# Kernel tuning notes

Measured on AMD Instinct MI355X. Metric: run time of the kernel, lower is better.

The kernel has to match this reference:

```python
import jax, jax.numpy as jnp
import numpy as np

HIDDEN = 1024
HEADS = 16
HEAD_DIM = HIDDEN // HEADS


def setup_inputs() -> dict:
    key = jax.random.key(0)
    ks = jax.random.split(key, 8)
    B, S = 2, 2048
    scale = 1.0 / np.sqrt(HIDDEN)
    inp = {
        "hidden_states": jax.random.normal(ks[0], (B, S, HIDDEN), dtype=jnp.float32),
        "attention_mask": jnp.zeros((B, 1, 1, S), dtype=jnp.float32),
        "q_w": jax.random.normal(ks[1], (HIDDEN, HIDDEN), dtype=jnp.float32) * scale,
        "q_b": jnp.zeros((HIDDEN,), dtype=jnp.float32),
        "k_w": jax.random.normal(ks[2], (HIDDEN, HIDDEN), dtype=jnp.float32) * scale,
        "k_b": jnp.zeros((HIDDEN,), dtype=jnp.float32),
        "v_w": jax.random.normal(ks[3], (HIDDEN, HIDDEN), dtype=jnp.float32) * scale,
        "v_b": jnp.zeros((HIDDEN,), dtype=jnp.float32),
    }
    return inp


def _split_heads(x):
    # [B, S, H] -> [B, heads, S, head_dim]
    B, S, _ = x.shape
    return x.reshape(B, S, HEADS, HEAD_DIM).transpose(0, 2, 1, 3)


def reference(hidden_states, attention_mask, q_w, q_b, k_w, k_b, v_w, v_b):
    # Linear projections (torch Linear: x @ W.T + b; here weights stored as [in, out])
    q = _split_heads(hidden_states @ q_w + q_b)  # [B, h, S, d]
    k = _split_heads(hidden_states @ k_w + k_b)
    v = _split_heads(hidden_states @ v_w + v_b)

    scores = jnp.einsum("bhqd,bhkd->bhqk", q, k) / jnp.sqrt(jnp.float32(HEAD_DIM))
    scores = scores + attention_mask  # additive mask, broadcast [B,1,1,S]
    probs = jax.nn.softmax(scores, axis=-1)
    # dropout prob = 0.0 -> identity
    ctx = jnp.einsum("bhqk,bhkd->bhqd", probs, v)  # [B, h, S, d]
    B, _, S, _ = ctx.shape
    ctx = ctx.transpose(0, 2, 1, 3).reshape(B, S, HIDDEN)
    return ctx
```

## Files before the change

### kernel.cpp

```cpp
#include <hip/hip_runtime.h>

typedef __bf16 bf16;
typedef __attribute__((ext_vector_type(8))) __bf16 bf16x8;
typedef __attribute__((ext_vector_type(4))) __bf16 bf16x4;
typedef __attribute__((ext_vector_type(4))) float f32x4;
typedef __attribute__((ext_vector_type(2))) unsigned int uint2v;
typedef __attribute__((ext_vector_type(4))) unsigned int uint4v;

#define MFMA(a, b, c) __builtin_amdgcn_mfma_f32_16x16x32_bf16((a), (b), (c), 0, 0, 0)
#define LOG2E 1.44269504088896340736f

__device__ __forceinline__ bf16x8 cvt8(float4 a, float4 b) {
  bf16x8 r;
  r[0] = (bf16)a.x; r[1] = (bf16)a.y; r[2] = (bf16)a.z; r[3] = (bf16)a.w;
  r[4] = (bf16)b.x; r[5] = (bf16)b.y; r[6] = (bf16)b.z; r[7] = (bf16)b.w;
  return r;
}

__device__ __forceinline__ void stage16(const bf16* g, bf16* l) {
  __builtin_amdgcn_global_load_lds(
      (const __attribute__((address_space(1))) void*)g,
      (__attribute__((address_space(3))) void*)l, 16, 0, 0);
}

__global__ __launch_bounds__(256)
void cvt(const float* __restrict__ hs, const float* __restrict__ qw,
         const float* __restrict__ kw, const float* __restrict__ vw,
         bf16* __restrict__ Xb, bf16* __restrict__ Wt) {
  const int bid = blockIdx.x, tid = threadIdx.x;
  if (bid < 2048) {
    size_t off = (size_t)bid * 2048 + tid * 8;
    float4 x0 = *(const float4*)(hs + off);
    float4 x1 = *(const float4*)(hs + off + 4);
    *(bf16x8*)(Xb + off) = cvt8(x0, x1);
  } else {
    int t = bid - 2048;
    int z = t >> 8, ti = t & 255;
    const float* W = (z == 0) ? qw : (z == 1) ? kw : vw;
    int k0 = (ti >> 4) * 64, n0 = (ti & 15) * 64;
    __shared__ bf16 T[64 * 72];
    #pragma unroll
    for (int i = 0; i < 16; ++i) {
      int e = i * 256 + tid;
      int kr = e >> 6, nc = e & 63;
      T[nc * 72 + kr] = (bf16)W[(size_t)(k0 + kr) * 1024 + n0 + nc];
    }
    __syncthreads();
    #pragma unroll
    for (int i = 0; i < 2; ++i) {
      int e = i * 256 + tid;
      int nr = e >> 3, kg = e & 7;
      *(bf16x8*)(Wt + (size_t)z * 1048576 + (size_t)(n0 + nr) * 1024 + k0 + kg * 8) =
          *(const bf16x8*)&T[nr * 72 + kg * 8];
    }
  }
}

__global__ __launch_bounds__(256, 3)
void qkv_gemm(const bf16* __restrict__ Xb, const bf16* __restrict__ Wt,
              const float* __restrict__ qbias, const float* __restrict__ kbias,
              const float* __restrict__ vbias,
              bf16* __restrict__ qo, bf16* __restrict__ ko, bf16* __restrict__ vo) {
  const int blk = blockIdx.x;
  const int xcd = blk & 7, slot = blk >> 3;
  const int mb = xcd * 4 + slot / 24;
  const int nb = slot % 24;
  const int z = nb >> 3, nbm = nb & 7;
  const bf16* W = Wt + (size_t)z * 1048576;

  const int tid = threadIdx.x;
  const int wave = tid >> 6, lane = tid & 63, quad = lane >> 4, c = lane & 15;
  const int wr = wave >> 1, wc = wave & 1;
  const int lrow = lane >> 3;
  const int lg = (lane & 7) ^ lrow;

  __shared__ bf16 As[128 * 64];
  __shared__ bf16 Bs[128 * 64];

  f32x4 acc[4][4] = {};

  for (int k0 = 0; k0 < 1024; k0 += 64) {
    #pragma unroll
    for (int i = 0; i < 4; ++i) {
      int r = wave * 32 + i * 8;
      stage16(Xb + (size_t)(mb * 128 + r + lrow) * 1024 + k0 + lg * 8, &As[r * 64]);
      stage16(W + (size_t)(nbm * 128 + r + lrow) * 1024 + k0 + lg * 8, &Bs[r * 64]);
    }
    __syncthreads();
    #pragma unroll
    for (int ch = 0; ch < 2; ++ch) {
      bf16x8 af[4];
      #pragma unroll
      for (int rt = 0; rt < 4; ++rt) {
        int row = wr * 64 + rt * 16 + c;
        af[rt] = *(const bf16x8*)&As[row * 64 + ((((ch << 2) | quad) ^ (c & 7)) << 3)];
      }
      #pragma unroll
      for (int nt = 0; nt < 4; ++nt) {
        int row = wc * 64 + nt * 16 + c;
        bf16x8 bfrag = *(const bf16x8*)&Bs[row * 64 + ((((ch << 2) | quad) ^ (c & 7)) << 3)];
        #pragma unroll
        for (int rt = 0; rt < 4; ++rt)
          acc[rt][nt] = MFMA(af[rt], bfrag, acc[rt][nt]);
      }
    }
    __syncthreads();
  }

  const float* bias = (z == 0) ? qbias : (z == 1) ? kbias : vbias;
  float bv[4];
  #pragma unroll
  for (int nt = 0; nt < 4; ++nt)
    bv[nt] = bias[nbm * 128 + wc * 64 + nt * 16 + c];

  if (z == 2) {
    #pragma unroll
    for (int rt = 0; rt < 4; ++rt)
      #pragma unroll
      for (int nt = 0; nt < 4; ++nt) {
        int m0 = mb * 128 + wr * 64 + rt * 16 + 4 * quad;
        int n = nbm * 128 + wc * 64 + nt * 16 + c;
        bf16x4 pk;
        #pragma unroll
        for (int reg = 0; reg < 4; ++reg) pk[reg] = (bf16)(acc[rt][nt][reg] + bv[nt]);
        int b = m0 >> 11, s0 = m0 & 2047, h = n >> 6, d = n & 63;
        *(bf16x4*)&vo[(((size_t)b * 16 + h) * 64 + d) * 2048 + s0] = pk;
      }
  } else {
    bf16* dst = (z == 0) ? qo : ko;
    const float scale = (z == 0) ? 0.125f * LOG2E : 1.0f;
    #pragma unroll
    for (int rt = 0; rt < 4; ++rt)
      #pragma unroll
      for (int nt = 0; nt < 4; ++nt)
        #pragma unroll
        for (int reg = 0; reg < 4; ++reg) {
          float v = (acc[rt][nt][reg] + bv[nt]) * scale;
          int m = mb * 128 + wr * 64 + rt * 16 + 4 * quad + reg;
          int n = nbm * 128 + wc * 64 + nt * 16 + c;
          int b = m >> 11, s = m & 2047, h = n >> 6, d = n & 63;
          dst[(((size_t)b * 16 + h) * 2048 + s) * 64 + d] = (bf16)v;
        }
  }
}

__global__ __launch_bounds__(256, 4)
void attn(const bf16* __restrict__ qg, const bf16* __restrict__ kg,
          const bf16* __restrict__ vtg, const float* __restrict__ mask,
          float* __restrict__ out) {
  const int blk = blockIdx.x;
  const int xcd = blk & 7, slot = blk >> 3;
  const int bh = xcd * 4 + (slot >> 5);
  const int qblk = slot & 31;
  const int b = bh >> 4, h = bh & 15;
  const int tid = threadIdx.x;
  const int wave = tid >> 6, lane = tid & 63, quad = lane >> 4, c = lane & 15;
  const int w2 = wave & 1;
  const int wq = wave >> 1;
  const int lrow = lane >> 3, lg = (lane & 7) ^ lrow;

  __shared__ __align__(16) unsigned char SH[40960];
  float* Ms = (float*)(SH + 32768);

  const bf16* qb_ = qg + (size_t)bh * 2048 * 64;
  const bf16* kb_ = kg + (size_t)bh * 2048 * 64;
  const bf16* vb_ = vtg + (size_t)bh * 64 * 2048;

  #pragma unroll
  for (int i = 0; i < 2; ++i) {
    int idx = i * 1024 + tid * 4;
    float4 m = *(const float4*)&mask[b * 2048 + idx];
    float4 ms = {m.x * LOG2E, m.y * LOG2E, m.z * LOG2E, m.w * LOG2E};
    *(float4*)&Ms[idx] = ms;
  }

  bf16x8 qf[2][2];
  #pragma unroll
  for (int g = 0; g < 2; ++g)
    #pragma unroll
    for (int ch = 0; ch < 2; ++ch)
      qf[g][ch] = *(const bf16x8*)(qb_ +
          (size_t)(qblk * 64 + wq * 32 + g * 16 + c) * 64 + ch * 32 + quad * 8);

  #pragma unroll
  for (int i = 0; i < 2; ++i) {
    int r = wave * 16 + i * 8;
    stage16(kb_ + (size_t)(r + lrow) * 64 + lg * 8, (bf16*)SH + r * 64);
    stage16(vb_ + (size_t)(r + lrow) * 2048 + lg * 8, (bf16*)(SH + 16384) + r * 64);
  }
  __asm__ volatile("s_waitcnt lgkmcnt(0)" ::: "memory");

  f32x4 o[4][2] = {};
  float lsum[2] = {0.f, 0.f};

  for (int kt = 0; kt < 32; ++kt) {
    const int cur = kt & 1;
    bf16* Kc = (bf16*)(SH + cur * 8192);
    bf16* Vc = (bf16*)(SH + 16384 + cur * 8192);
    __asm__ volatile("s_waitcnt vmcnt(0)" ::: "memory");
    __builtin_amdgcn_s_barrier();
    __builtin_amdgcn_sched_barrier(0);

    if (kt < 31) {
      bf16* Kn = (bf16*)(SH + (cur ^ 1) * 8192);
      bf16* Vn = (bf16*)(SH + 16384 + (cur ^ 1) * 8192);
      #pragma unroll
      for (int i = 0; i < 2; ++i) {
        int r = wave * 16 + i * 8;
        stage16(kb_ + (size_t)((kt + 1) * 64 + r + lrow) * 64 + lg * 8, Kn + r * 64);
        stage16(vb_ + (size_t)(r + lrow) * 2048 + (kt + 1) * 64 + lg * 8, Vn + r * 64);
      }
    }
    __builtin_amdgcn_sched_barrier(0);

    f32x4 s[2][2];
    #pragma unroll
    for (int kt2 = 0; kt2 < 2; ++kt2) {
      float4 mv = *(const float4*)&Ms[kt * 64 + w2 * 32 + kt2 * 16 + 4 * quad];
      f32x4 sv = {mv.x, mv.y, mv.z, mv.w};
      s[0][kt2] = sv;
      s[1][kt2] = sv;
    }

    __builtin_amdgcn_s_setprio(1);
    #pragma unroll
    for (int kt2 = 0; kt2 < 2; ++kt2)
      #pragma unroll
      for (int ch = 0; ch < 2; ++ch) {
        bf16x8 kf = *(const bf16x8*)&Kc[(w2 * 32 + kt2 * 16 + c) * 64 +
                                        ((((ch << 2) | quad) ^ (c & 7)) << 3)];
        s[0][kt2] = MFMA(kf, qf[0][ch], s[0][kt2]);
        s[1][kt2] = MFMA(kf, qf[1][ch], s[1][kt2]);
      }
    __builtin_amdgcn_s_setprio(0);

    bf16x8 pf[2];
    #pragma unroll
    for (int g = 0; g < 2; ++g) {
      unsigned int A0, A1, B0, B1;
      {
        bf16x4 pk;
        #pragma unroll
        for (int reg = 0; reg < 4; ++reg) {
          float p = __builtin_amdgcn_exp2f(s[g][0][reg]);
          lsum[g] += p;
          pk[reg] = (bf16)p;
        }
        uint2v uu = __builtin_bit_cast(uint2v, pk);
        A0 = uu.x; A1 = uu.y;
      }
      {
        bf16x4 pk;
        #pragma unroll
        for (int reg = 0; reg < 4; ++reg) {
          float p = __builtin_amdgcn_exp2f(s[g][1][reg]);
          lsum[g] += p;
          pk[reg] = (bf16)p;
        }
        uint2v uu = __builtin_bit_cast(uint2v, pk);
        B0 = uu.x; B1 = uu.y;
      }
      __asm__ volatile("v_permlane32_swap_b32 %0, %1" : "+v"(A0), "+v"(B0));
      __asm__ volatile("v_permlane32_swap_b32 %0, %1" : "+v"(A1), "+v"(B1));
      __asm__ volatile("v_permlane16_swap_b32 %0, %1" : "+v"(A0), "+v"(B0));
      __asm__ volatile("v_permlane16_swap_b32 %0, %1" : "+v"(A1), "+v"(B1));
      uint4v up = {A0, A1, B0, B1};
      pf[g] = __builtin_bit_cast(bf16x8, up);
    }

    __builtin_amdgcn_s_setprio(1);
    #pragma unroll
    for (int dt = 0; dt < 4; ++dt) {
      bf16x8 vf = *(const bf16x8*)&Vc[(dt * 16 + c) * 64 +
                                      ((((w2 << 2) | quad) ^ (c & 7)) << 3)];
      o[dt][0] = MFMA(vf, pf[0], o[dt][0]);
      o[dt][1] = MFMA(vf, pf[1], o[dt][1]);
    }
    __builtin_amdgcn_s_setprio(0);
  }

  #pragma unroll
  for (int g = 0; g < 2; ++g) {
    lsum[g] += __shfl_xor(lsum[g], 16, 64);
    lsum[g] += __shfl_xor(lsum[g], 32, 64);
  }

  __syncthreads();
  float* rec = (float*)(SH + (size_t)(wq * 64 + lane) * 144);
  if (w2 == 1) {
    #pragma unroll
    for (int dt = 0; dt < 4; ++dt)
      #pragma unroll
      for (int g = 0; g < 2; ++g)
        *(f32x4*)&rec[(dt * 2 + g) * 4] = o[dt][g];
    rec[32] = lsum[0];
    rec[33] = lsum[1];
  }
  __syncthreads();
  if (w2 == 0) {
    float inv[2];
    #pragma unroll
    for (int g = 0; g < 2; ++g) inv[g] = 1.0f / (lsum[g] + rec[32 + g]);
    #pragma unroll
    for (int dt = 0; dt < 4; ++dt)
      #pragma unroll
      for (int g = 0; g < 2; ++g) {
        f32x4 po = *(const f32x4*)&rec[(dt * 2 + g) * 4];
        const int srow = qblk * 64 + wq * 32 + g * 16 + c;
        float4 st = { (o[dt][g][0] + po[0]) * inv[g],
                      (o[dt][g][1] + po[1]) * inv[g],
                      (o[dt][g][2] + po[2]) * inv[g],
                      (o[dt][g][3] + po[3]) * inv[g] };
        *(float4*)&out[((size_t)b * 2048 + srow) * 1024 + h * 64 + dt * 16 + 4 * quad] = st;
      }
  }
}

extern "C" void kernel_launch(void* const* d_in, const int* in_sizes, int n_in,
                              void* d_out, int out_size, void* d_ws, size_t ws_size,
                              hipStream_t stream) {
  const float* hs   = (const float*)d_in[0];
  const float* mask = (const float*)d_in[1];
  const float* qw   = (const float*)d_in[2];
  const float* qb   = (const float*)d_in[3];
  const float* kw   = (const float*)d_in[4];
  const float* kb   = (const float*)d_in[5];
  const float* vw   = (const float*)d_in[6];
  const float* vb   = (const float*)d_in[7];
  float* out = (float*)d_out;

  bf16* Xb   = (bf16*)d_ws;
  bf16* Wt   = Xb + (size_t)4096 * 1024;
  bf16* q_ws = Wt + (size_t)3 * 1048576;
  bf16* k_ws = q_ws + (size_t)4096 * 1024;
  bf16* v_ws = k_ws + (size_t)4096 * 1024;

  cvt<<<dim3(2816), 256, 0, stream>>>(hs, qw, kw, vw, Xb, Wt);
  qkv_gemm<<<dim3(768), 256, 0, stream>>>(Xb, Wt, qb, kb, vb, q_ws, k_ws, v_ws);
  attn<<<dim3(1024), 256, 0, stream>>>(q_ws, k_ws, v_ws, mask, out);
}
```

Baseline: 161.3 us.

## Load K/V fragments straight from global into registers, drop LDS staging

Rewrites the attention kernel so each wave loads its K, V and mask fragments directly from global memory into registers, double-buffered in two register sets, with no LDS staging or barriers. Each wave now covers all keys for 32 query rows, which removes the split-K reduction through shared memory, and the grid is halved to 512 blocks of 128 query rows each. The aim is to remove barrier and LDS traffic. The cost is that each wave re-reads K/V from global/L2 with no sharing across the block, plus higher register pressure and fewer blocks in flight.

```diff
diff --git a/kernel.cpp b/kernel.cpp
--- a/kernel.cpp
+++ b/kernel.cpp
@@ -144,35 +144,28 @@
   }
 }
 
-__global__ __launch_bounds__(256, 4)
+struct Frags {
+  bf16x8 k[4];
+  bf16x8 v[4];
+  float4 m[2];
+};
+
+__global__ __launch_bounds__(256, 1)
 void attn(const bf16* __restrict__ qg, const bf16* __restrict__ kg,
           const bf16* __restrict__ vtg, const float* __restrict__ mask,
           float* __restrict__ out) {
   const int blk = blockIdx.x;
-  const int xcd = blk & 7, slot = blk >> 3;
-  const int bh = xcd * 4 + (slot >> 5);
-  const int qblk = slot & 31;
+  const int xcd = blk & 7;
+  const int bh = xcd * 4 + ((blk >> 3) & 3);
+  const int qsup = blk >> 5;
   const int b = bh >> 4, h = bh & 15;
   const int tid = threadIdx.x;
   const int wave = tid >> 6, lane = tid & 63, quad = lane >> 4, c = lane & 15;
-  const int w2 = wave & 1;
-  const int wq = wave >> 1;
-  const int lrow = lane >> 3, lg = (lane & 7) ^ lrow;
-
-  __shared__ __align__(16) unsigned char SH[40960];
-  float* Ms = (float*)(SH + 32768);
 
   const bf16* qb_ = qg + (size_t)bh * 2048 * 64;
   const bf16* kb_ = kg + (size_t)bh * 2048 * 64;
   const bf16* vb_ = vtg + (size_t)bh * 64 * 2048;
-
-  #pragma unroll
-  for (int i = 0; i < 2; ++i) {
-    int idx = i * 1024 + tid * 4;
-    float4 m = *(const float4*)&mask[b * 2048 + idx];
-    float4 ms = {m.x * LOG2E, m.y * LOG2E, m.z * LOG2E, m.w * LOG2E};
-    *(float4*)&Ms[idx] = ms;
-  }
+  const float* mb_ = mask + (size_t)b * 2048;
 
   bf16x8 qf[2][2];
   #pragma unroll
@@ -180,60 +173,47 @@
     #pragma unroll
     for (int ch = 0; ch < 2; ++ch)
       qf[g][ch] = *(const bf16x8*)(qb_ +
-          (size_t)(qblk * 64 + wq * 32 + g * 16 + c) * 64 + ch * 32 + quad * 8);
-
-  #pragma unroll
-  for (int i = 0; i < 2; ++i) {
-    int r = wave * 16 + i * 8;
-    stage16(kb_ + (size_t)(r + lrow) * 64 + lg * 8, (bf16*)SH + r * 64);
-    stage16(vb_ + (size_t)(r + lrow) * 2048 + lg * 8, (bf16*)(SH + 16384) + r * 64);
-  }
-  __asm__ volatile("s_waitcnt lgkmcnt(0)" ::: "memory");
+          (size_t)(qsup * 128 + wave * 32 + g * 16 + c) * 64 + ch * 32 + quad * 8);
 
   f32x4 o[4][2] = {};
   float lsum[2] = {0.f, 0.f};
 
-  for (int kt = 0; kt < 32; ++kt) {
-    const int cur = kt & 1;
-    bf16* Kc = (bf16*)(SH + cur * 8192);
-    bf16* Vc = (bf16*)(SH + 16384 + cur * 8192);
-    __asm__ volatile("s_waitcnt vmcnt(0)" ::: "memory");
-    __builtin_amdgcn_s_barrier();
-    __builtin_amdgcn_sched_barrier(0);
-
-    if (kt < 31) {
-      bf16* Kn = (bf16*)(SH + (cur ^ 1) * 8192);
-      bf16* Vn = (bf16*)(SH + 16384 + (cur ^ 1) * 8192);
-      #pragma unroll
-      for (int i = 0; i < 2; ++i) {
-        int r = wave * 16 + i * 8;
-        stage16(kb_ + (size_t)((kt + 1) * 64 + r + lrow) * 64 + lg * 8, Kn + r * 64);
-        stage16(vb_ + (size_t)(r + lrow) * 2048 + (kt + 1) * 64 + lg * 8, Vn + r * 64);
-      }
-    }
-    __builtin_amdgcn_sched_barrier(0);
-
+  Frags fA, fB;
+
+  auto LOADF = [&](Frags& f, int kt) {
+    #pragma unroll
+    for (int kt2 = 0; kt2 < 2; ++kt2)
+      #pragma unroll
+      for (int ch = 0; ch < 2; ++ch)
+        f.k[kt2 * 2 + ch] = *(const bf16x8*)(kb_ +
+            (size_t)(kt * 32 + kt2 * 16 + c) * 64 + (ch * 4 + quad) * 8);
+    #pragma unroll
+    for (int dt = 0; dt < 4; ++dt)
+      f.v[dt] = *(const bf16x8*)(vb_ +
+          (size_t)(dt * 16 + c) * 2048 + kt * 32 + quad * 8);
+    #pragma unroll
+    for (int kt2 = 0; kt2 < 2; ++kt2)
+      f.m[kt2] = *(const float4*)(mb_ + kt * 32 + kt2 * 16 + 4 * quad);
+  };
+
+  auto COMPUTE = [&](const Frags& f) {
     f32x4 s[2][2];
     #pragma unroll
     for (int kt2 = 0; kt2 < 2; ++kt2) {
-      float4 mv = *(const float4*)&Ms[kt * 64 + w2 * 32 + kt2 * 16 + 4 * quad];
-      f32x4 sv = {mv.x, mv.y, mv.z, mv.w};
+      f32x4 sv = {f.m[kt2].x * LOG2E, f.m[kt2].y * LOG2E,
+                  f.m[kt2].z * LOG2E, f.m[kt2].w * LOG2E};
       s[0][kt2] = sv;
       s[1][kt2] = sv;
     }
-
     __builtin_amdgcn_s_setprio(1);
     #pragma unroll
     for (int kt2 = 0; kt2 < 2; ++kt2)
       #pragma unroll
       for (int ch = 0; ch < 2; ++ch) {
-        bf16x8 kf = *(const bf16x8*)&Kc[(w2 * 32 + kt2 * 16 + c) * 64 +
-                                        ((((ch << 2) | quad) ^ (c & 7)) << 3)];
-        s[0][kt2] = MFMA(kf, qf[0][ch], s[0][kt2]);
-        s[1][kt2] = MFMA(kf, qf[1][ch], s[1][kt2]);
+        s[0][kt2] = MFMA(f.k[kt2 * 2 + ch], qf[0][ch], s[0][kt2]);
+        s[1][kt2] = MFMA(f.k[kt2 * 2 + ch], qf[1][ch], s[1][kt2]);
       }
     __builtin_amdgcn_s_setprio(0);
-
     bf16x8 pf[2];
     #pragma unroll
     for (int g = 0; g < 2; ++g) {
@@ -267,52 +247,36 @@
       uint4v up = {A0, A1, B0, B1};
       pf[g] = __builtin_bit_cast(bf16x8, up);
     }
-
     __builtin_amdgcn_s_setprio(1);
     #pragma unroll
     for (int dt = 0; dt < 4; ++dt) {
-      bf16x8 vf = *(const bf16x8*)&Vc[(dt * 16 + c) * 64 +
-                                      ((((w2 << 2) | quad) ^ (c & 7)) << 3)];
-      o[dt][0] = MFMA(vf, pf[0], o[dt][0]);
-      o[dt][1] = MFMA(vf, pf[1], o[dt][1]);
+      o[dt][0] = MFMA(f.v[dt], pf[0], o[dt][0]);
+      o[dt][1] = MFMA(f.v[dt], pf[1], o[dt][1]);
     }
     __builtin_amdgcn_s_setprio(0);
+  };
+
+  LOADF(fA, 0);
+  for (int kt = 0; kt < 64; kt += 2) {
+    LOADF(fB, kt + 1);
+    COMPUTE(fA);
+    if (kt + 2 < 64) LOADF(fA, kt + 2);
+    COMPUTE(fB);
   }
 
   #pragma unroll
   for (int g = 0; g < 2; ++g) {
-    lsum[g] += __shfl_xor(lsum[g], 16, 64);
-    lsum[g] += __shfl_xor(lsum[g], 32, 64);
-  }
-
-  __syncthreads();
-  float* rec = (float*)(SH + (size_t)(wq * 64 + lane) * 144);
-  if (w2 == 1) {
-    #pragma unroll
-    for (int dt = 0; dt < 4; ++dt)
-      #pragma unroll
-      for (int g = 0; g < 2; ++g)
-        *(f32x4*)&rec[(dt * 2 + g) * 4] = o[dt][g];
-    rec[32] = lsum[0];
-    rec[33] = lsum[1];
-  }
-  __syncthreads();
-  if (w2 == 0) {
-    float inv[2];
-    #pragma unroll
-    for (int g = 0; g < 2; ++g) inv[g] = 1.0f / (lsum[g] + rec[32 + g]);
-    #pragma unroll
-    for (int dt = 0; dt < 4; ++dt)
-      #pragma unroll
-      for (int g = 0; g < 2; ++g) {
-        f32x4 po = *(const f32x4*)&rec[(dt * 2 + g) * 4];
-        const int srow = qblk * 64 + wq * 32 + g * 16 + c;
-        float4 st = { (o[dt][g][0] + po[0]) * inv[g],
-                      (o[dt][g][1] + po[1]) * inv[g],
-                      (o[dt][g][2] + po[2]) * inv[g],
-                      (o[dt][g][3] + po[3]) * inv[g] };
-        *(float4*)&out[((size_t)b * 2048 + srow) * 1024 + h * 64 + dt * 16 + 4 * quad] = st;
-      }
+    float l = lsum[g];
+    l += __shfl_xor(l, 16, 64);
+    l += __shfl_xor(l, 32, 64);
+    const float inv = 1.0f / l;
+    const int srow = qsup * 128 + wave * 32 + g * 16 + c;
+    #pragma unroll
+    for (int dt = 0; dt < 4; ++dt) {
+      float4 st = { o[dt][g][0] * inv, o[dt][g][1] * inv,
+                    o[dt][g][2] * inv, o[dt][g][3] * inv };
+      *(float4*)&out[((size_t)b * 2048 + srow) * 1024 + h * 64 + dt * 16 + 4 * quad] = st;
+    }
   }
 }
 
@@ -337,5 +301,5 @@
 
   cvt<<<dim3(2816), 256, 0, stream>>>(hs, qw, kw, vw, Xb, Wt);
   qkv_gemm<<<dim3(768), 256, 0, stream>>>(Xb, Wt, qb, kb, vb, q_ws, k_ws, v_ws);
-  attn<<<dim3(1024), 256, 0, stream>>>(q_ws, k_ws, v_ws, mask, out);
-}
+  attn<<<dim3(512), 256, 0, stream>>>(q_ws, k_ws, v_ws, mask, out);
+}
```

New measurement: 236.7 us. 46.7% more time.

## Double-buffer QKV GEMM LDS tiles with BK=32 and prefetch next tile

Applied to the files above, without the earlier changes.

Replaces the single-buffered 64-wide K tile in the QKV projection GEMM with two 32-wide LDS buffers. The load of tile k+1 is issued before computing tile k, and there is one barrier per iteration instead of two. The XOR swizzle is adjusted to the 32-element row layout. This aims to overlap global-to-LDS loads with MFMA work, but it doubles the iteration count and issues a full vmcnt(0) wait every step.

```diff
diff --git a/kernel.cpp b/kernel.cpp
--- a/kernel.cpp
+++ b/kernel.cpp
@@ -71,40 +71,53 @@
   const int tid = threadIdx.x;
   const int wave = tid >> 6, lane = tid & 63, quad = lane >> 4, c = lane & 15;
   const int wr = wave >> 1, wc = wave & 1;
-  const int lrow = lane >> 3;
-  const int lg = (lane & 7) ^ lrow;
-
-  __shared__ bf16 As[128 * 64];
-  __shared__ bf16 Bs[128 * 64];
+  const int srow = lane >> 2;
+  const int spos = lane & 3;
+
+  __shared__ bf16 As[2][128 * 32];
+  __shared__ bf16 Bs[2][128 * 32];
 
   f32x4 acc[4][4] = {};
 
-  for (int k0 = 0; k0 < 1024; k0 += 64) {
-    #pragma unroll
-    for (int i = 0; i < 4; ++i) {
-      int r = wave * 32 + i * 8;
-      stage16(Xb + (size_t)(mb * 128 + r + lrow) * 1024 + k0 + lg * 8, &As[r * 64]);
-      stage16(W + (size_t)(nbm * 128 + r + lrow) * 1024 + k0 + lg * 8, &Bs[r * 64]);
-    }
-    __syncthreads();
-    #pragma unroll
-    for (int ch = 0; ch < 2; ++ch) {
-      bf16x8 af[4];
-      #pragma unroll
-      for (int rt = 0; rt < 4; ++rt) {
-        int row = wr * 64 + rt * 16 + c;
-        af[rt] = *(const bf16x8*)&As[row * 64 + ((((ch << 2) | quad) ^ (c & 7)) << 3)];
-      }
-      #pragma unroll
-      for (int nt = 0; nt < 4; ++nt) {
-        int row = wc * 64 + nt * 16 + c;
-        bf16x8 bfrag = *(const bf16x8*)&Bs[row * 64 + ((((ch << 2) | quad) ^ (c & 7)) << 3)];
-        #pragma unroll
-        for (int rt = 0; rt < 4; ++rt)
-          acc[rt][nt] = MFMA(af[rt], bfrag, acc[rt][nt]);
-      }
-    }
-    __syncthreads();
+  auto STAGE = [&](int kt, int buf) {
+    #pragma unroll
+    for (int i = 0; i < 2; ++i) {
+      int rbase = wave * 32 + i * 16;
+      int r = rbase + srow;
+      int g = spos ^ ((r >> 1) & 3);
+      stage16(Xb + (size_t)(mb * 128 + r) * 1024 + kt * 32 + g * 8,
+              &As[buf][rbase * 32]);
+      stage16(W + (size_t)(nbm * 128 + r) * 1024 + kt * 32 + g * 8,
+              &Bs[buf][rbase * 32]);
+    }
+  };
+
+  STAGE(0, 0);
+  for (int kt = 0; kt < 32; ++kt) {
+    const int buf = kt & 1;
+    __asm__ volatile("s_waitcnt vmcnt(0)" ::: "memory");
+    __builtin_amdgcn_s_barrier();
+    __builtin_amdgcn_sched_barrier(0);
+
+    if (kt < 31) STAGE(kt + 1, buf ^ 1);
+    __builtin_amdgcn_sched_barrier(0);
+
+    bf16x8 af[4];
+    #pragma unroll
+    for (int rt = 0; rt < 4; ++rt) {
+      int row = wr * 64 + rt * 16 + c;
+      af[rt] = *(const bf16x8*)&As[buf][row * 32 +
+                                        ((quad ^ ((c >> 1) & 3)) << 3)];
+    }
+    #pragma unroll
+    for (int nt = 0; nt < 4; ++nt) {
+      int row = wc * 64 + nt * 16 + c;
+      bf16x8 bfrag = *(const bf16x8*)&Bs[buf][row * 32 +
+                                             ((quad ^ ((c >> 1) & 3)) << 3)];
+      #pragma unroll
+      for (int rt = 0; rt < 4; ++rt)
+        acc[rt][nt] = MFMA(af[rt], bfrag, acc[rt][nt]);
+    }
   }
 
   const float* bias = (z == 0) ? qbias : (z == 1) ? kbias : vbias;
```

New measurement: 168.2 us. +4.3%, slower.
